# Performance work log

Measured on AMD Instinct MI355X. Metric: run time of the kernel, lower is better.

The kernel has to match this reference:

```python
import jax, jax.numpy as jnp
import numpy as np

VOCAB, EMBED, UNITS = 32000, 512, 1024
B, T = 32, 128


def setup_inputs() -> dict:
    key = jax.random.key(0)
    ks = jax.random.split(key, 8)
    g = lambda k, shape, s: jax.random.normal(k, shape, jnp.float32) * s
    return {
        "tokens": jax.random.randint(ks[0], (B, T), 0, VOCAB),
        "emb_table": g(ks[1], (VOCAB, EMBED), 0.02),
        "kernel_f": g(ks[2], (EMBED, 3 * UNITS), 0.02),
        "rec_kernel_f": g(ks[3], (UNITS, 3 * UNITS), 0.02),
        "bias_f": g(ks[4], (2, 3 * UNITS), 0.02),
        "kernel_b": g(ks[5], (EMBED, 3 * UNITS), 0.02),
        "rec_kernel_b": g(ks[6], (UNITS, 3 * UNITS), 0.02),
        "bias_b": g(ks[7], (2, 3 * UNITS), 0.02),
    }


def _gru(x, kernel, rec_kernel, bias, reverse):
    # Keras GRU, reset_after=True. x: [B,T,E] -> outputs [B,T,U], final state [B,U]
    units = rec_kernel.shape[0]
    x_proj = jnp.einsum('bte,eu->btu', x, kernel) + bias[0]  # input-side gates, all timesteps
    xp = jnp.swapaxes(x_proj, 0, 1)  # [T,B,3U] for scan
    h0 = jnp.zeros((x.shape[0], units), x.dtype)

    def step(h, xpt):
        rec = h @ rec_kernel + bias[1]
        xz, xr, xh = jnp.split(xpt, 3, axis=-1)
        rz, rr, rh = jnp.split(rec, 3, axis=-1)
        z = jax.nn.sigmoid(xz + rz)          # update gate
        r = jax.nn.sigmoid(xr + rr)          # reset gate
        hh = jnp.tanh(xh + r * rh)           # candidate (reset applied after recurrent matmul)
        hn = z * h + (1.0 - z) * hh
        return hn, hn

    hT, ys = jax.lax.scan(step, h0, xp, reverse=reverse)
    return jnp.swapaxes(ys, 0, 1), hT  # outputs back to [B,T,U]


def reference(tokens, emb_table, kernel_f, rec_kernel_f, bias_f, kernel_b, rec_kernel_b, bias_b):
    x = emb_table[tokens]  # [B,T,E]
    yf, hf = _gru(x, kernel_f, rec_kernel_f, bias_f, reverse=False)
    yb, hb = _gru(x, kernel_b, rec_kernel_b, bias_b, reverse=True)  # Bidirectional backward dir
    return yf + yb, hf, hb  # merge_mode='sum', states [h_forward, h_backward]
```

## Files before the change

kernel.cpp:

```cpp
#include <hip/hip_runtime.h>


using u16 = unsigned short;
using u32 = unsigned int;
typedef __attribute__((ext_vector_type(8))) short bfx8;
typedef __attribute__((ext_vector_type(4))) float f32x4;
typedef __attribute__((ext_vector_type(4))) u32 u32x4;
typedef __attribute__((ext_vector_type(3))) u32 u32x3;
typedef __attribute__((ext_vector_type(4))) u16 u16x4;

#define B_ 32
#define T_ 128
#define E_ 512
#define U_ 1024
#define NG 3072
#define M_ 4096
#define YN 4194304
#define ROTB 131072
#define HXD  393216

__device__ __forceinline__ float bf2f(u16 u) {
  union { u32 i; float f; } v; v.i = (u32)u << 16; return v.f;
}
__device__ __forceinline__ u16 f2bf(float f) {
  union { float f; u32 i; } v; v.f = f;
  u32 r = v.i + 0x7FFFu + ((v.i >> 16) & 1u);
  return (u16)(r >> 16);
}
__device__ __forceinline__ float sigm(float x) { return 1.0f / (1.0f + __expf(-x)); }

__device__ __forceinline__ void load_lds16(const void* g, void* l) {
  __builtin_amdgcn_global_load_lds(
      (const __attribute__((address_space(1))) u32*)g,
      (__attribute__((address_space(3))) u32*)l, 16, 0, 0);
}

__global__ __launch_bounds__(256) void k_embed(const int* __restrict__ tok,
                                               const float* __restrict__ emb,
                                               u16* __restrict__ X) {
  int idx = blockIdx.x * 256 + threadIdx.x;
  int m = idx >> 6, k8 = (idx & 63) << 3;
  int b = m & 31, t = m >> 5;
  int tk = tok[b * T_ + t];
  const float* s = emb + (size_t)tk * E_ + k8;
  float4 v0 = *(const float4*)s, v1 = *(const float4*)(s + 4);
  bfx8 r;
  r[0]=(short)f2bf(v0.x); r[1]=(short)f2bf(v0.y); r[2]=(short)f2bf(v0.z); r[3]=(short)f2bf(v0.w);
  r[4]=(short)f2bf(v1.x); r[5]=(short)f2bf(v1.y); r[6]=(short)f2bf(v1.z); r[7]=(short)f2bf(v1.w);
  *(bfx8*)(X + (size_t)m * E_ + k8) = r;
}

__global__ void k_transpose(const float* __restrict__ in, u16* __restrict__ out,
                            int K, int N, int remap) {
  __shared__ float tile[32][33];
  int k0 = blockIdx.x * 32, n0 = blockIdx.y * 32;
  int tx = threadIdx.x, ty = threadIdx.y;
  for (int j = ty; j < 32; j += 8) tile[j][tx] = in[(size_t)(k0 + j) * N + n0 + tx];
  __syncthreads();
  for (int j = ty; j < 32; j += 8) {
    int n = n0 + j;
    int row = remap ? ((((n & 1023) >> 5) * 96) + ((n >> 10) << 5) + (n & 31)) : n;
    out[(size_t)row * K + k0 + tx] = f2bf(tile[tx][j]);
  }
}

__global__ __launch_bounds__(256) void k_xproj(const u16* __restrict__ X,
                                               const u16* __restrict__ WT,
                                               const float* __restrict__ biasF,
                                               const float* __restrict__ biasB,
                                               u16* __restrict__ XP) {
  const int n0 = blockIdx.x * 128, m0 = blockIdx.y * 128, dir = blockIdx.z;
  const float* bias = dir ? biasB : biasF;
  const u16* Wd = WT + (size_t)dir * NG * E_;
  __shared__ __align__(16) u16 As[128 * 64];
  __shared__ __align__(16) u16 Bs[128 * 64];
  const int tid = threadIdx.x;
  const int wave = tid >> 6, lane = tid & 63;
  const int moff = (wave >> 1) * 64, noff = (wave & 1) * 64;
  const int l15 = lane & 15, l4 = lane >> 4;
  f32x4 acc[4][4] = {};
  for (int kt = 0; kt < 8; ++kt) {
    int k0 = kt * 64;
#pragma unroll
    for (int j = 0; j < 4; ++j) {
      int o = j * 4096 + tid * 16;
      int row = o >> 7;
      int kk = (((o & 127) ^ ((row & 7) << 4)) >> 1);
      load_lds16(X  + (size_t)(m0 + row) * E_ + k0 + kk, (char*)As + o);
      load_lds16(Wd + (size_t)(n0 + row) * E_ + k0 + kk, (char*)Bs + o);
    }
    __syncthreads();
#pragma unroll
    for (int Ks = 0; Ks < 2; ++Ks) {
      bfx8 a[4], b[4];
#pragma unroll
      for (int Mt = 0; Mt < 4; ++Mt) {
        int ra = moff + Mt * 16 + l15;
        int ba = (ra << 7) + ((Ks * 32 + l4 * 8) << 1);
        ba ^= (ra & 7) << 4;
        a[Mt] = *(const bfx8*)((const char*)As + ba);
      }
#pragma unroll
      for (int Nt = 0; Nt < 4; ++Nt) {
        int rb = noff + Nt * 16 + l15;
        int bb2 = (rb << 7) + ((Ks * 32 + l4 * 8) << 1);
        bb2 ^= (rb & 7) << 4;
        b[Nt] = *(const bfx8*)((const char*)Bs + bb2);
      }
#pragma unroll
      for (int Mt = 0; Mt < 4; ++Mt)
#pragma unroll
        for (int Nt = 0; Nt < 4; ++Nt)
          acc[Mt][Nt] = __builtin_amdgcn_mfma_f32_16x16x32_bf16(a[Mt], b[Nt], acc[Mt][Nt], 0, 0, 0);
    }
    __syncthreads();
  }
  float bv[4];
#pragma unroll
  for (int Nt = 0; Nt < 4; ++Nt) bv[Nt] = bias[n0 + noff + Nt * 16 + l15];
#pragma unroll
  for (int Mt = 0; Mt < 4; ++Mt)
#pragma unroll
    for (int Nt = 0; Nt < 4; ++Nt)
#pragma unroll
      for (int r = 0; r < 4; ++r) {
        int m = m0 + moff + Mt * 16 + l4 * 4 + r;
        int n = n0 + noff + Nt * 16 + l15;
        XP[((size_t)dir * M_ + m) * NG + n] = f2bf(acc[Mt][Nt][r] + bv[Nt]);
      }
}

__global__ __launch_bounds__(256, 1) void k_gru(
    const u16* __restrict__ RW,
    u16* __restrict__ XP,
    const float* __restrict__ bf_, const float* __restrict__ bb_,
    char* __restrict__ Hx,
    float* __restrict__ out) {
  const int tid = threadIdx.x;
  const int wave = tid >> 6, lane = tid & 63;
  const int wg = blockIdx.x;
  const int dir = wg & 1, slice = wg >> 1;
  const int u0 = slice * 32;
  const float* b1p = (dir ? bb_ : bf_) + NG;
  const u16* wbase = RW + (size_t)dir * NG * U_ + (size_t)slice * 96 * U_;
  u16* xpd = XP + (size_t)dir * M_ * NG;
  char* hxd = Hx + (size_t)dir * HXD;
  __shared__ float pl[4][32][97];

  const int l15 = lane & 15, l4 = lane >> 4;

  bfx8 wf[6][8];
#pragma unroll
  for (int Nt = 0; Nt < 6; ++Nt)
#pragma unroll
    for (int Ks = 0; Ks < 8; ++Ks) {
      int c = Nt * 16 + l15;
      int k = wave * 256 + Ks * 32 + l4 * 8;
      wf[Nt][Ks] = *(const bfx8*)(wbase + (size_t)c * U_ + k);
    }

  const int eb = tid & 31;
  const int ug = tid >> 5;
  const int uu = ug * 4;
  float b1[3][4];
#pragma unroll
  for (int g = 0; g < 3; ++g)
#pragma unroll
    for (int j = 0; j < 4; ++j) b1[g][j] = b1p[g * U_ + u0 + uu + j];
  float hreg[4] = {0.f, 0.f, 0.f, 0.f};

  const int offb = wave * 32768 + l4 * 1024 + l15 * 16;
  const int sp = wave * 8 + (lane & 7);
  const int poff = (8 * sp + 7) * 512 + 31 * 16 + 8;
  const int soff = (slice * 8 + ug) * 512 + eb * 16;

  u16x4 xc[3];
  {
    int t0 = dir ? 127 : 0;
    const u16* xr = xpd + (size_t)(t0 * 32 + eb) * NG + u0 + uu;
#pragma unroll
    for (int g = 0; g < 3; ++g) xc[g] = *(const u16x4*)(xr + g * U_);
  }

  int rl = 0, rs = 1;
  for (int e = 0; e < 128; ++e) {
    f32x4 acc[2][6] = {};
    if (e > 0) {
      const u32 etag = (u32)e;
      char* rbase = hxd + rl * ROTB;
      {
        const char* pa = rbase + poff;
        u32 tv = etag;
        int g = 0;
        while (1) {
          if (lane < 8) {
            asm volatile("global_load_dword %0, %1, off sc0 sc1\n\ts_waitcnt vmcnt(0)"
                         : "=v"(tv) : "v"(pa));
          }
          if (__all((int)(tv == etag))) break;
          if (++g > (1 << 20)) break;
          __builtin_amdgcn_s_sleep(1);
        }
      }
      u32x3 L[2][8][2];
      int guard = 0;
      while (1) {
#pragma unroll
        for (int Ks = 0; Ks < 8; ++Ks) {
          const char* a = rbase + offb + Ks * 4096;
          asm volatile("global_load_dwordx3 %0, %1, off sc0 sc1"             : "=v"(L[0][Ks][0]) : "v"(a));
          asm volatile("global_load_dwordx3 %0, %1, off offset:512 sc0 sc1" : "=v"(L[0][Ks][1]) : "v"(a));
          asm volatile("global_load_dwordx3 %0, %1, off offset:256 sc0 sc1" : "=v"(L[1][Ks][0]) : "v"(a));
          asm volatile("global_load_dwordx3 %0, %1, off offset:768 sc0 sc1" : "=v"(L[1][Ks][1]) : "v"(a));
        }
        asm volatile("s_waitcnt vmcnt(0)");
#pragma unroll
        for (int Mt = 0; Mt < 2; ++Mt)
#pragma unroll
          for (int Ks = 0; Ks < 8; ++Ks)
            asm volatile("" : "+v"(L[Mt][Ks][0]), "+v"(L[Mt][Ks][1]));
        u32 bad = 0;
#pragma unroll
        for (int Mt = 0; Mt < 2; ++Mt)
#pragma unroll
          for (int Ks = 0; Ks < 8; ++Ks)
            bad |= (L[Mt][Ks][0].z ^ etag) | (L[Mt][Ks][1].z ^ etag);
        if (__all((int)(bad == 0))) break;
        if (++guard > (1 << 18)) break;
        __builtin_amdgcn_s_sleep(1);
      }
      bfx8 af[2][8];
#pragma unroll
      for (int Mt = 0; Mt < 2; ++Mt)
#pragma unroll
        for (int Ks = 0; Ks < 8; ++Ks) {
          u32x4 fv = {L[Mt][Ks][0].x, L[Mt][Ks][0].y, L[Mt][Ks][1].x, L[Mt][Ks][1].y};
          af[Mt][Ks] = __builtin_bit_cast(bfx8, fv);
        }
      u16x4 xn[3];
      bool pf = (e < 127);
      if (pf) {
        int tn = dir ? (126 - e) : (e + 1);
        const u16* xr = xpd + (size_t)(tn * 32 + eb) * NG + u0 + uu;
#pragma unroll
        for (int g = 0; g < 3; ++g) xn[g] = *(const u16x4*)(xr + g * U_);
      }
      __builtin_amdgcn_sched_barrier(0);
#pragma unroll
      for (int Ks = 0; Ks < 8; ++Ks)
#pragma unroll
        for (int Mt = 0; Mt < 2; ++Mt)
#pragma unroll
          for (int Nt = 0; Nt < 6; ++Nt)
            acc[Mt][Nt] = __builtin_amdgcn_mfma_f32_16x16x32_bf16(af[Mt][Ks], wf[Nt][Ks],
                                                                  acc[Mt][Nt], 0, 0, 0);
      if (pf) {
      }
#pragma unroll
      for (int Mt = 0; Mt < 2; ++Mt)
#pragma unroll
        for (int Nt = 0; Nt < 6; ++Nt)
#pragma unroll
          for (int r = 0; r < 4; ++r)
            pl[wave][Mt * 16 + l4 * 4 + r][Nt * 16 + l15] = acc[Mt][Nt][r];
      __syncthreads();
      float hold[4];
#pragma unroll
      for (int j = 0; j < 4; ++j) hold[j] = hreg[j];
#pragma unroll
      for (int j = 0; j < 4; ++j) {
        int c = uu + j;
        float rz = pl[0][eb][c]      + pl[1][eb][c]      + pl[2][eb][c]      + pl[3][eb][c];
        float rr = pl[0][eb][32 + c] + pl[1][eb][32 + c] + pl[2][eb][32 + c] + pl[3][eb][32 + c];
        float rh = pl[0][eb][64 + c] + pl[1][eb][64 + c] + pl[2][eb][64 + c] + pl[3][eb][64 + c];
        float z  = sigm(bf2f(xc[0][j]) + rz + b1[0][j]);
        float r  = sigm(bf2f(xc[1][j]) + rr + b1[1][j]);
        float hh = tanhf(bf2f(xc[2][j]) + r * (rh + b1[2][j]));
        hreg[j] = z * hreg[j] + (1.f - z) * hh;
      }
      {
        u32 p01 = (u32)f2bf(hreg[0]) | ((u32)f2bf(hreg[1]) << 16);
        u32 p23 = (u32)f2bf(hreg[2]) | ((u32)f2bf(hreg[3]) << 16);
        u32x3 sv; sv.x = p01; sv.y = p23; sv.z = (u32)(e + 1);
        char* sa = hxd + rs * ROTB + soff;
        asm volatile("global_store_dwordx3 %0, %1, off sc0 sc1" :: "v"(sa), "v"(sv));
      }
      {
        const int tp = dir ? (128 - e) : (e - 1);
        float* yrow = (float*)(xpd + (size_t)(tp * 32 + eb) * NG);
        *(float4*)(yrow + u0 + uu) = make_float4(hold[0], hold[1], hold[2], hold[3]);
      }
      if (pf) { xc[0] = xn[0]; xc[1] = xn[1]; xc[2] = xn[2]; }
    } else {
      u16x4 xn[3];
      {
        int tn = dir ? 126 : 1;
        const u16* xr = xpd + (size_t)(tn * 32 + eb) * NG + u0 + uu;
#pragma unroll
        for (int g = 0; g < 3; ++g) xn[g] = *(const u16x4*)(xr + g * U_);
      }
#pragma unroll
      for (int j = 0; j < 4; ++j) {
        float z  = sigm(bf2f(xc[0][j]) + b1[0][j]);
        float r  = sigm(bf2f(xc[1][j]) + b1[1][j]);
        float hh = tanhf(bf2f(xc[2][j]) + r * b1[2][j]);
        hreg[j] = (1.f - z) * hh;
      }
      {
        u32 p01 = (u32)f2bf(hreg[0]) | ((u32)f2bf(hreg[1]) << 16);
        u32 p23 = (u32)f2bf(hreg[2]) | ((u32)f2bf(hreg[3]) << 16);
        u32x3 sv; sv.x = p01; sv.y = p23; sv.z = 1u;
        char* sa = hxd + rs * ROTB + soff;
        asm volatile("global_store_dwordx3 %0, %1, off sc0 sc1" :: "v"(sa), "v"(sv));
      }
      xc[0] = xn[0]; xc[1] = xn[1]; xc[2] = xn[2];
    }
    rl = rs; rs = (rs == 2) ? 0 : rs + 1;
    __syncthreads();
  }
  {
    const char* pa = hxd + 2 * ROTB + (8 * (lane & 31) + 7) * 512 + 31 * 16 + 8;
    u32 tv = 128u;
    int g = 0;
    while (1) {
      if (lane < 32) {
        asm volatile("global_load_dword %0, %1, off sc0 sc1\n\ts_waitcnt vmcnt(0)"
                     : "=v"(tv) : "v"(pa));
      }
      if (__all((int)(tv == 128u))) break;
      if (++g > (1 << 22)) break;
      __builtin_amdgcn_s_sleep(1);
    }
    const int tl = dir ? 0 : 127;
    float* yrow = (float*)(xpd + (size_t)(tl * 32 + eb) * NG);
    *(float4*)(yrow + u0 + uu) = make_float4(hreg[0], hreg[1], hreg[2], hreg[3]);
    float* os = out + YN + (size_t)dir * (B_ * U_) + (size_t)eb * U_ + u0 + uu;
    *(float4*)os = make_float4(hreg[0], hreg[1], hreg[2], hreg[3]);
  }
}

__global__ __launch_bounds__(256) void k_merge(const u16* __restrict__ XP,
                                               float* __restrict__ out) {
  int idx = blockIdx.x * 256 + threadIdx.x;
  int u4 = (idx & 255) * 4;
  int m = idx >> 8;
  int t = m >> 5, b = m & 31;
  const float* yf = (const float*)(XP + (size_t)m * NG);
  const float* yb = (const float*)(XP + (size_t)(M_ + m) * NG);
  float4 a = *(const float4*)(yf + u4);
  float4 c = *(const float4*)(yb + u4);
  float4 o; o.x = a.x + c.x; o.y = a.y + c.y; o.z = a.z + c.z; o.w = a.w + c.w;
  *(float4*)(out + ((size_t)b * T_ + t) * U_ + u4) = o;
}

extern "C" void kernel_launch(void* const* d_in, const int* in_sizes, int n_in,
                              void* d_out, int out_size, void* d_ws, size_t ws_size,
                              hipStream_t stream) {
  const int*   tokens = (const int*)d_in[0];
  const float* emb    = (const float*)d_in[1];
  const float* kf     = (const float*)d_in[2];
  const float* rkf    = (const float*)d_in[3];
  const float* bf_    = (const float*)d_in[4];
  const float* kb     = (const float*)d_in[5];
  const float* rkb    = (const float*)d_in[6];
  const float* bb_    = (const float*)d_in[7];
  float* out = (float*)d_out;
  char* ws = (char*)d_ws;

  u16*  X  = (u16*)ws;
  u16*  WT = (u16*)(ws + 0x400000);
  char* Hx = ws + 0x400000;
  u16*  RW = (u16*)(ws + 0xA00000);
  u16*  XP = (u16*)(ws + 0x1600000);

  k_embed<<<1024, 256, 0, stream>>>(tokens, emb, X);
  k_transpose<<<dim3(16, 96), dim3(32, 8), 0, stream>>>(kf,  WT,               512,  NG, 0);
  k_transpose<<<dim3(16, 96), dim3(32, 8), 0, stream>>>(kb,  WT + 3072 * 512,  512,  NG, 0);
  k_transpose<<<dim3(32, 96), dim3(32, 8), 0, stream>>>(rkf, RW,               1024, NG, 1);
  k_transpose<<<dim3(32, 96), dim3(32, 8), 0, stream>>>(rkb, RW + 3072 * 1024, 1024, NG, 1);
  k_xproj<<<dim3(24, 32, 2), 256, 0, stream>>>(X, WT, bf_, bb_, XP);
  hipMemsetAsync(Hx, 0, 2 * HXD, stream);
  k_gru<<<64, 256, 0, stream>>>(RW, XP, bf_, bb_, Hx, out);
  k_merge<<<4096, 256, 0, stream>>>(XP, out);
}
```

Before: 644.5 us.

## Drop pre-poll flag spin and switch hidden-state exchange to dwordx4 tagged records

Removes the separate single-flag polling loop before each step's hidden-state fetch and relies only on the per-record epoch tags checked in the bulk load loop. Hidden-state records now use 16-byte stores and loads (tag duplicated in the fourth word) instead of 12-byte ones, and the load order is rearranged so each dwordx4 feeds one fragment half. The gate epilogue is unified for the first and later steps, and tanhf is replaced with an exp-based tanh. The aim is lower per-step latency on the serial recurrence. The trade-off is that the bulk loads may now spin more often on data that is not yet ready, and the fast tanh may lose accuracy for large inputs.

```diff
diff --git a/kernel.cpp b/kernel.cpp
--- a/kernel.cpp
+++ b/kernel.cpp
@@ -6,7 +6,6 @@
 typedef __attribute__((ext_vector_type(8))) short bfx8;
 typedef __attribute__((ext_vector_type(4))) float f32x4;
 typedef __attribute__((ext_vector_type(4))) u32 u32x4;
-typedef __attribute__((ext_vector_type(3))) u32 u32x3;
 typedef __attribute__((ext_vector_type(4))) u16 u16x4;
 
 #define B_ 32
@@ -28,6 +27,10 @@
   return (u16)(r >> 16);
 }
 __device__ __forceinline__ float sigm(float x) { return 1.0f / (1.0f + __expf(-x)); }
+__device__ __forceinline__ float ftanh(float x) {
+  float e = __expf(2.f * x);
+  return 1.f - 2.f / (e + 1.f);
+}
 
 __device__ __forceinline__ void load_lds16(const void* g, void* l) {
   __builtin_amdgcn_global_load_lds(
@@ -170,8 +173,6 @@
   float hreg[4] = {0.f, 0.f, 0.f, 0.f};
 
   const int offb = wave * 32768 + l4 * 1024 + l15 * 16;
-  const int sp = wave * 8 + (lane & 7);
-  const int poff = (8 * sp + 7) * 512 + 31 * 16 + 8;
   const int soff = (slice * 8 + ug) * 512 + eb * 16;
 
   u16x4 xc[3];
@@ -185,61 +186,46 @@
   int rl = 0, rs = 1;
   for (int e = 0; e < 128; ++e) {
     f32x4 acc[2][6] = {};
+    u16x4 xn[3] = {xc[0], xc[1], xc[2]};
     if (e > 0) {
       const u32 etag = (u32)e;
       char* rbase = hxd + rl * ROTB;
-      {
-        const char* pa = rbase + poff;
-        u32 tv = etag;
-        int g = 0;
-        while (1) {
-          if (lane < 8) {
-            asm volatile("global_load_dword %0, %1, off sc0 sc1\n\ts_waitcnt vmcnt(0)"
-                         : "=v"(tv) : "v"(pa));
-          }
-          if (__all((int)(tv == etag))) break;
-          if (++g > (1 << 20)) break;
-          __builtin_amdgcn_s_sleep(1);
-        }
-      }
-      u32x3 L[2][8][2];
+      u32x4 L[2][8], L2[2][8];
       int guard = 0;
       while (1) {
 #pragma unroll
         for (int Ks = 0; Ks < 8; ++Ks) {
           const char* a = rbase + offb + Ks * 4096;
-          asm volatile("global_load_dwordx3 %0, %1, off sc0 sc1"             : "=v"(L[0][Ks][0]) : "v"(a));
-          asm volatile("global_load_dwordx3 %0, %1, off offset:512 sc0 sc1" : "=v"(L[0][Ks][1]) : "v"(a));
-          asm volatile("global_load_dwordx3 %0, %1, off offset:256 sc0 sc1" : "=v"(L[1][Ks][0]) : "v"(a));
-          asm volatile("global_load_dwordx3 %0, %1, off offset:768 sc0 sc1" : "=v"(L[1][Ks][1]) : "v"(a));
+          asm volatile("global_load_dwordx4 %0, %1, off sc0 sc1"             : "=v"(L[0][Ks])  : "v"(a));
+          asm volatile("global_load_dwordx4 %0, %1, off offset:256 sc0 sc1" : "=v"(L2[0][Ks]) : "v"(a));
+          asm volatile("global_load_dwordx4 %0, %1, off offset:512 sc0 sc1" : "=v"(L[1][Ks])  : "v"(a));
+          asm volatile("global_load_dwordx4 %0, %1, off offset:768 sc0 sc1" : "=v"(L2[1][Ks]) : "v"(a));
         }
         asm volatile("s_waitcnt vmcnt(0)");
 #pragma unroll
-        for (int Mt = 0; Mt < 2; ++Mt)
+        for (int h = 0; h < 2; ++h)
 #pragma unroll
           for (int Ks = 0; Ks < 8; ++Ks)
-            asm volatile("" : "+v"(L[Mt][Ks][0]), "+v"(L[Mt][Ks][1]));
+            asm volatile("" : "+v"(L[h][Ks]), "+v"(L2[h][Ks]));
         u32 bad = 0;
 #pragma unroll
-        for (int Mt = 0; Mt < 2; ++Mt)
+        for (int h = 0; h < 2; ++h)
 #pragma unroll
           for (int Ks = 0; Ks < 8; ++Ks)
-            bad |= (L[Mt][Ks][0].z ^ etag) | (L[Mt][Ks][1].z ^ etag);
+            bad |= (L[h][Ks].z ^ etag) | (L2[h][Ks].z ^ etag);
         if (__all((int)(bad == 0))) break;
         if (++guard > (1 << 18)) break;
         __builtin_amdgcn_s_sleep(1);
       }
       bfx8 af[2][8];
 #pragma unroll
-      for (int Mt = 0; Mt < 2; ++Mt)
-#pragma unroll
-        for (int Ks = 0; Ks < 8; ++Ks) {
-          u32x4 fv = {L[Mt][Ks][0].x, L[Mt][Ks][0].y, L[Mt][Ks][1].x, L[Mt][Ks][1].y};
-          af[Mt][Ks] = __builtin_bit_cast(bfx8, fv);
-        }
-      u16x4 xn[3];
-      bool pf = (e < 127);
-      if (pf) {
+      for (int Ks = 0; Ks < 8; ++Ks) {
+        u32x4 f0 = {L[0][Ks].x, L[0][Ks].y, L[1][Ks].x, L[1][Ks].y};
+        u32x4 f1 = {L2[0][Ks].x, L2[0][Ks].y, L2[1][Ks].x, L2[1][Ks].y};
+        af[0][Ks] = __builtin_bit_cast(bfx8, f0);
+        af[1][Ks] = __builtin_bit_cast(bfx8, f1);
+      }
+      if (e < 127) {
         int tn = dir ? (126 - e) : (e + 1);
         const u16* xr = xpd + (size_t)(tn * 32 + eb) * NG + u0 + uu;
 #pragma unroll
@@ -254,78 +240,60 @@
           for (int Nt = 0; Nt < 6; ++Nt)
             acc[Mt][Nt] = __builtin_amdgcn_mfma_f32_16x16x32_bf16(af[Mt][Ks], wf[Nt][Ks],
                                                                   acc[Mt][Nt], 0, 0, 0);
-      if (pf) {
-      }
-#pragma unroll
-      for (int Mt = 0; Mt < 2; ++Mt)
-#pragma unroll
-        for (int Nt = 0; Nt < 6; ++Nt)
-#pragma unroll
-          for (int r = 0; r < 4; ++r)
-            pl[wave][Mt * 16 + l4 * 4 + r][Nt * 16 + l15] = acc[Mt][Nt][r];
-      __syncthreads();
-      float hold[4];
-#pragma unroll
-      for (int j = 0; j < 4; ++j) hold[j] = hreg[j];
-#pragma unroll
-      for (int j = 0; j < 4; ++j) {
-        int c = uu + j;
-        float rz = pl[0][eb][c]      + pl[1][eb][c]      + pl[2][eb][c]      + pl[3][eb][c];
-        float rr = pl[0][eb][32 + c] + pl[1][eb][32 + c] + pl[2][eb][32 + c] + pl[3][eb][32 + c];
-        float rh = pl[0][eb][64 + c] + pl[1][eb][64 + c] + pl[2][eb][64 + c] + pl[3][eb][64 + c];
-        float z  = sigm(bf2f(xc[0][j]) + rz + b1[0][j]);
-        float r  = sigm(bf2f(xc[1][j]) + rr + b1[1][j]);
-        float hh = tanhf(bf2f(xc[2][j]) + r * (rh + b1[2][j]));
-        hreg[j] = z * hreg[j] + (1.f - z) * hh;
-      }
-      {
-        u32 p01 = (u32)f2bf(hreg[0]) | ((u32)f2bf(hreg[1]) << 16);
-        u32 p23 = (u32)f2bf(hreg[2]) | ((u32)f2bf(hreg[3]) << 16);
-        u32x3 sv; sv.x = p01; sv.y = p23; sv.z = (u32)(e + 1);
-        char* sa = hxd + rs * ROTB + soff;
-        asm volatile("global_store_dwordx3 %0, %1, off sc0 sc1" :: "v"(sa), "v"(sv));
-      }
-      {
-        const int tp = dir ? (128 - e) : (e - 1);
-        float* yrow = (float*)(xpd + (size_t)(tp * 32 + eb) * NG);
-        *(float4*)(yrow + u0 + uu) = make_float4(hold[0], hold[1], hold[2], hold[3]);
-      }
-      if (pf) { xc[0] = xn[0]; xc[1] = xn[1]; xc[2] = xn[2]; }
     } else {
-      u16x4 xn[3];
-      {
-        int tn = dir ? 126 : 1;
-        const u16* xr = xpd + (size_t)(tn * 32 + eb) * NG + u0 + uu;
-#pragma unroll
-        for (int g = 0; g < 3; ++g) xn[g] = *(const u16x4*)(xr + g * U_);
-      }
-#pragma unroll
-      for (int j = 0; j < 4; ++j) {
-        float z  = sigm(bf2f(xc[0][j]) + b1[0][j]);
-        float r  = sigm(bf2f(xc[1][j]) + b1[1][j]);
-        float hh = tanhf(bf2f(xc[2][j]) + r * b1[2][j]);
-        hreg[j] = (1.f - z) * hh;
-      }
-      {
-        u32 p01 = (u32)f2bf(hreg[0]) | ((u32)f2bf(hreg[1]) << 16);
-        u32 p23 = (u32)f2bf(hreg[2]) | ((u32)f2bf(hreg[3]) << 16);
-        u32x3 sv; sv.x = p01; sv.y = p23; sv.z = 1u;
-        char* sa = hxd + rs * ROTB + soff;
-        asm volatile("global_store_dwordx3 %0, %1, off sc0 sc1" :: "v"(sa), "v"(sv));
-      }
-      xc[0] = xn[0]; xc[1] = xn[1]; xc[2] = xn[2];
-    }
+      int tn = dir ? 126 : 1;
+      const u16* xr = xpd + (size_t)(tn * 32 + eb) * NG + u0 + uu;
+#pragma unroll
+      for (int g = 0; g < 3; ++g) xn[g] = *(const u16x4*)(xr + g * U_);
+    }
+#pragma unroll
+    for (int Mt = 0; Mt < 2; ++Mt)
+#pragma unroll
+      for (int Nt = 0; Nt < 6; ++Nt)
+#pragma unroll
+        for (int r = 0; r < 4; ++r)
+          pl[wave][Mt * 16 + l4 * 4 + r][Nt * 16 + l15] = acc[Mt][Nt][r];
+    __syncthreads();
+    float hold[4];
+#pragma unroll
+    for (int j = 0; j < 4; ++j) hold[j] = hreg[j];
+#pragma unroll
+    for (int j = 0; j < 4; ++j) {
+      int c = uu + j;
+      float rz = pl[0][eb][c]      + pl[1][eb][c]      + pl[2][eb][c]      + pl[3][eb][c];
+      float rr = pl[0][eb][32 + c] + pl[1][eb][32 + c] + pl[2][eb][32 + c] + pl[3][eb][32 + c];
+      float rh = pl[0][eb][64 + c] + pl[1][eb][64 + c] + pl[2][eb][64 + c] + pl[3][eb][64 + c];
+      float z  = sigm(bf2f(xc[0][j]) + rz + b1[0][j]);
+      float r  = sigm(bf2f(xc[1][j]) + rr + b1[1][j]);
+      float hh = ftanh(bf2f(xc[2][j]) + r * (rh + b1[2][j]));
+      hreg[j] = z * hreg[j] + (1.f - z) * hh;
+    }
+    {
+      u32 p01 = (u32)f2bf(hreg[0]) | ((u32)f2bf(hreg[1]) << 16);
+      u32 p23 = (u32)f2bf(hreg[2]) | ((u32)f2bf(hreg[3]) << 16);
+      u32x4 sv; sv.x = p01; sv.y = p23; sv.z = (u32)(e + 1); sv.w = (u32)(e + 1);
+      char* sa = hxd + rs * ROTB + soff;
+      asm volatile("global_store_dwordx4 %0, %1, off sc0 sc1" :: "v"(sa), "v"(sv));
+    }
+    if (e > 0) {
+      const int tp = dir ? (128 - e) : (e - 1);
+      float* yrow = (float*)(xpd + (size_t)(tp * 32 + eb) * NG);
+      *(float4*)(yrow + u0 + uu) = make_float4(hold[0], hold[1], hold[2], hold[3]);
+    }
+    xc[0] = xn[0]; xc[1] = xn[1]; xc[2] = xn[2];
     rl = rs; rs = (rs == 2) ? 0 : rs + 1;
     __syncthreads();
   }
   {
-    const char* pa = hxd + 2 * ROTB + (8 * (lane & 31) + 7) * 512 + 31 * 16 + 8;
-    u32 tv = 128u;
+    const char* pa = hxd + 2 * ROTB + ((lane & 31) * 8 + 7) * 512 + 31 * 16;
     int g = 0;
     while (1) {
+      u32 tv = 128u;
       if (lane < 32) {
-        asm volatile("global_load_dword %0, %1, off sc0 sc1\n\ts_waitcnt vmcnt(0)"
-                     : "=v"(tv) : "v"(pa));
+        u32x4 tvv;
+        asm volatile("global_load_dwordx4 %0, %1, off sc0 sc1\n\ts_waitcnt vmcnt(0)"
+                     : "=v"(tvv) : "v"(pa));
+        tv = tvv.z;
       }
       if (__all((int)(tv == 128u))) break;
       if (++g > (1 << 22)) break;
```

Result: faster. 627.0 us (-2.7%).
